# Optimization experiments

Hardware: AMD Instinct MI355X
Metric: run time of the kernel (lower is better)

## Reference

```python
import jax, jax.numpy as jnp
import numpy as np

OUT_FEATURES = 4096
IN_FEATURES = 4096
SCALE_EPS = 1e-5


def setup_inputs() -> dict:
    key = jax.random.key(0)
    k1, k2, k3 = jax.random.split(key, 3)
    x = jax.random.normal(k1, (8192, IN_FEATURES), dtype=jnp.float32)
    # packed int4 weights: two signed nibbles per byte-equivalent int
    weight_packed = jax.random.randint(k2, (OUT_FEATURES, IN_FEATURES // 2), 0, 256, dtype=jnp.int32)
    weight_scale = jax.random.uniform(k3, (OUT_FEATURES,), dtype=jnp.float32) * 0.01 + 1e-4
    return {"x": x, "weight_packed": weight_packed, "weight_scale": weight_scale}


def _unpack_int4(weight_packed):
    # low nibble first, then high nibble, sign-extended from 4 bits
    low = weight_packed & 15
    high = (weight_packed >> 4) & 15
    low = jnp.where(low > 7, low - 16, low)
    high = jnp.where(high > 7, high - 16, high)
    # interleave -> [out_features, in_features]
    w_q = jnp.stack([low, high], axis=-1).reshape(weight_packed.shape[0], -1)
    return w_q


def reference(x, weight_packed, weight_scale):
    # per-row activation quantization to int4 range [-8, 7]
    x_max = jnp.max(jnp.abs(x), axis=-1, keepdims=True)
    x_scale = jnp.maximum(x_max / 7.0, SCALE_EPS)          # [tokens, 1]
    x_q = jnp.clip(jnp.round(x / x_scale), -8.0, 7.0)      # float carrier of int4 values

    w_q = _unpack_int4(weight_packed).astype(jnp.float32)  # [out, in]

    out = jnp.einsum('ti,oi->to', x_q, w_q)                # [tokens, out]
    out = out * (x_scale * weight_scale[None, :])
    return out.astype(x.dtype)
```

## Files before the change

### kernel.cpp

```cpp
#include <hip/hip_runtime.h>

#define SCALE_EPS 1e-5f

typedef int v4i __attribute__((ext_vector_type(4)));

static __device__ __forceinline__ void gll16(const void* g, void* l) {
  __builtin_amdgcn_global_load_lds(
      (const __attribute__((address_space(1))) unsigned int*)g,
      (__attribute__((address_space(3))) unsigned int*)l,
      16, 0, 0);
}

__global__ __launch_bounds__(256) void unpack_w(const int* __restrict__ wp,
                                                char* __restrict__ wq) {
  const int kc = blockIdx.x;
  const int nt = blockIdx.y;
  const int tid = threadIdx.x;
  char* tile = wq + ((size_t)nt * 64 + kc) * 8192;
  const int n0 = nt * 128;
#pragma unroll
  for (int j = 0; j < 4; ++j) {
    int u = j * 256 + tid;
    int r = u >> 3;
    int p = u & 7;
    const v4i* src = (const v4i*)((const char*)wp + (size_t)(n0 + r) * 8192 + kc * 128 + p * 16);
    v4i v = *src;
    unsigned int b[8];
#pragma unroll
    for (int q = 0; q < 4; ++q) {
      int lo = ((v[q] & 15) ^ 8) - 8;
      int hi = (((v[q] >> 4) & 15) ^ 8) - 8;
      b[q * 2]     = (unsigned int)(lo & 255);
      b[q * 2 + 1] = (unsigned int)(hi & 255);
    }
    unsigned int w0 = b[0] | (b[1] << 8) | (b[2] << 16) | (b[3] << 24);
    unsigned int w1 = b[4] | (b[5] << 8) | (b[6] << 16) | (b[7] << 24);
    *(uint2*)(tile + (r >> 4) * 1024 + (p >> 1) * 256 + (r & 15) * 16 + (p & 1) * 8) =
        make_uint2(w0, w1);
  }
}

__global__ __launch_bounds__(256) void quant_x(const float* __restrict__ x,
                                               char* __restrict__ xq,
                                               float* __restrict__ xs) {
  __shared__ float lmax[4][4];
  const int tid = threadIdx.x;
  const int w = tid >> 6;
  const int l = tid & 63;
  const int t0 = blockIdx.x * 4;
  const int row = l >> 4;
  const int t = t0 + row;
  const int sub = l & 15;

  const float* base = x + (size_t)t * 4096 + w * 1024 + sub * 4;
  float4 vals[16];
  float m = 0.0f;
#pragma unroll
  for (int s = 0; s < 16; ++s) {
    vals[s] = *(const float4*)(base + s * 64);
    m = fmaxf(m, fmaxf(fmaxf(fabsf(vals[s].x), fabsf(vals[s].y)),
                       fmaxf(fabsf(vals[s].z), fabsf(vals[s].w))));
  }
#pragma unroll
  for (int d = 1; d < 16; d <<= 1) m = fmaxf(m, __shfl_xor(m, d, 64));
  if (sub == 0) lmax[w][row] = m;
  __syncthreads();
  float rm = fmaxf(fmaxf(lmax[0][row], lmax[1][row]),
                   fmaxf(lmax[2][row], lmax[3][row]));
  float scale = fmaxf(rm / 7.0f, SCALE_EPS);
  if (w == 0 && sub == 0) xs[t] = scale;

  const int mt = t0 >> 7;
  const int f = (t0 & 127) >> 4;
  const int r16 = t & 15;
  const int cc = sub >> 2;
  const int b4 = (sub & 3) * 4;

#pragma unroll
  for (int s = 0; s < 16; ++s) {
    float4 v = vals[s];
    int q0 = (int)fminf(fmaxf(rintf(v.x / scale), -8.0f), 7.0f);
    int q1 = (int)fminf(fmaxf(rintf(v.y / scale), -8.0f), 7.0f);
    int q2 = (int)fminf(fmaxf(rintf(v.z / scale), -8.0f), 7.0f);
    int q3 = (int)fminf(fmaxf(rintf(v.w / scale), -8.0f), 7.0f);
    unsigned int wd = (unsigned int)(q0 & 255) | ((unsigned int)(q1 & 255) << 8) |
                      ((unsigned int)(q2 & 255) << 16) | ((unsigned int)(q3 & 255) << 24);
    *(unsigned int*)(xq + ((size_t)mt * 64 + w * 16 + s) * 8192 +
                     f * 1024 + cc * 256 + r16 * 16 + b4) = wd;
  }
}

__global__ __launch_bounds__(512, 2) void gemm_i8(const char* __restrict__ xq,
                                                  const char* __restrict__ wq,
                                                  const float* __restrict__ xs,
                                                  const float* __restrict__ wsc,
                                                  float* __restrict__ out) {
  __shared__ char lds[4][32768];
  const int tid = threadIdx.x;
  const int wid = tid >> 6;
  const int lane = tid & 63;
  const int wm = wid >> 2;
  const int wn = wid & 3;

  const int bid = blockIdx.x;
  const int wg = (bid & 7) * 64 + (bid >> 3);
  const int by = wg >> 4;
  const int bx = wg & 15;

  const char* Asrc0 = xq + (size_t)(2 * by) * 64 * 8192;
  const char* Asrc1 = Asrc0 + 64 * 8192;
  const char* Bsrc0 = wq + (size_t)(2 * bx) * 64 * 8192;
  const char* Bsrc1 = Bsrc0 + 64 * 8192;
  const int toff = tid * 16;

  v4i acc[8][4] = {};
  v4i fA[2][8], fB[2][4];

#define STAGE4(kt)                                                      \
  do {                                                                  \
    char* dst_ = lds[(kt) & 3] + toff;                                  \
    gll16(Asrc0 + (size_t)(kt) * 8192 + toff, dst_);                    \
    gll16(Asrc1 + (size_t)(kt) * 8192 + toff, dst_ + 8192);             \
    gll16(Bsrc0 + (size_t)(kt) * 8192 + toff, dst_ + 16384);            \
    gll16(Bsrc1 + (size_t)(kt) * 8192 + toff, dst_ + 24576);            \
  } while (0)

#define LOADFRAGS(n, kt1)                                               \
  do {                                                                  \
    const char* As_ = lds[(kt1) & 3] + wm * 8192 + lane * 16;           \
    const char* Bs_ = lds[(kt1) & 3] + 16384 + wn * 4096 + lane * 16;   \
    _Pragma("unroll") for (int mi = 0; mi < 8; ++mi)                    \
        fA[n][mi] = *(const v4i*)(As_ + mi * 1024);                     \
    _Pragma("unroll") for (int ni = 0; ni < 4; ++ni)                    \
        fB[n][ni] = *(const v4i*)(Bs_ + ni * 1024);                     \
  } while (0)

#define MFMAC(c)                                                        \
  do {                                                                  \
    __builtin_amdgcn_s_setprio(1);                                      \
    _Pragma("unroll") for (int mi = 0; mi < 8; ++mi)                    \
        _Pragma("unroll") for (int ni = 0; ni < 4; ++ni)                \
            acc[mi][ni] = __builtin_amdgcn_mfma_i32_16x16x64_i8(        \
                fA[c][mi], fB[c][ni], acc[mi][ni], 0, 0, 0);            \
    __builtin_amdgcn_s_setprio(0);                                      \
  } while (0)

#define ITER(c, n, kt, do_stage, vm)                                    \
  do {                                                                  \
    if (do_stage) STAGE4((kt) + 3);                                     \
    LOADFRAGS(n, (kt) + 1);                                             \
    __builtin_amdgcn_sched_barrier(0);                                  \
    MFMAC(c);                                                           \
    asm volatile("s_waitcnt lgkmcnt(0)" ::: "memory");                  \
    if ((vm) == 4) asm volatile("s_waitcnt vmcnt(4)" ::: "memory");     \
    else if ((vm) == 0) asm volatile("s_waitcnt vmcnt(0)" ::: "memory");\
    __builtin_amdgcn_sched_barrier(0);                                  \
    __builtin_amdgcn_s_barrier();                                       \
    __builtin_amdgcn_sched_barrier(0);                                  \
  } while (0)

  STAGE4(0); STAGE4(1); STAGE4(2);
  asm volatile("s_waitcnt vmcnt(8)" ::: "memory");
  __builtin_amdgcn_s_barrier();
  __builtin_amdgcn_sched_barrier(0);
  LOADFRAGS(0, 0);
  asm volatile("s_waitcnt vmcnt(4) lgkmcnt(0)" ::: "memory");
  __builtin_amdgcn_sched_barrier(0);
  __builtin_amdgcn_s_barrier();
  __builtin_amdgcn_sched_barrier(0);

  for (int kt = 0; kt < 60; kt += 2) {
    ITER(0, 1, kt, true, 4);
    ITER(1, 0, kt + 1, true, 4);
  }
  ITER(0, 1, 60, true, 4);
  ITER(1, 0, 61, false, 0);
  ITER(0, 1, 62, false, -1);
  MFMAC(1);

#undef ITER
#undef MFMAC
#undef LOADFRAGS
#undef STAGE4

  float wvv[4];
#pragma unroll
  for (int ni = 0; ni < 4; ++ni)
    wvv[ni] = wsc[bx * 256 + wn * 64 + ni * 16 + (lane & 15)];
  const int rbase = by * 256 + wm * 128 + ((lane >> 4) << 2);
  const int cbase = bx * 256 + wn * 64 + (lane & 15);
#pragma unroll
  for (int mi = 0; mi < 8; ++mi) {
#pragma unroll
    for (int j = 0; j < 4; ++j) {
      int t = rbase + mi * 16 + j;
      float xsv = xs[t];
      float* orow = out + (size_t)t * 4096 + cbase;
#pragma unroll
      for (int ni = 0; ni < 4; ++ni)
        orow[ni * 16] = (float)acc[mi][ni][j] * (xsv * wvv[ni]);
    }
  }
}

extern "C" void kernel_launch(void* const* d_in, const int* in_sizes, int n_in,
                              void* d_out, int out_size, void* d_ws, size_t ws_size,
                              hipStream_t stream) {
  const float* x = (const float*)d_in[0];
  const int* wp = (const int*)d_in[1];
  const float* wsc = (const float*)d_in[2];
  float* out = (float*)d_out;
  char* ws = (char*)d_ws;

  char* xq = ws;
  char* wq = ws + 33554432;
  float* xs = (float*)(ws + 33554432 + 16777216);

  hipLaunchKernelGGL(unpack_w, dim3(64, 32), dim3(256), 0, stream, wp, wq);
  hipLaunchKernelGGL(quant_x, dim3(2048), dim3(256), 0, stream, x, xq, xs);
  hipLaunchKernelGGL(gemm_i8, dim3(512), dim3(512), 0, stream, xq, wq, xs, wsc, out);
}
```

Measured before the change: 176.0 us.

## Stream A fragments in pairs interleaved with MFMAs in the int8 GEMM loop

After: 172.8 us. Within noise of the previous version (-1.8%).

```diff
diff --git a/kernel.cpp b/kernel.cpp
--- a/kernel.cpp
+++ b/kernel.cpp
@@ -114,7 +114,8 @@
   const int toff = tid * 16;
 
   v4i acc[8][4] = {};
-  v4i fA[2][8], fB[2][4];
+  v4i fB[2][4];
+  v4i aA0, aA1, aA2, aA3;
 
 #define STAGE4(kt)                                                      \
   do {                                                                  \
@@ -125,62 +126,81 @@
     gll16(Bsrc1 + (size_t)(kt) * 8192 + toff, dst_ + 24576);            \
   } while (0)
 
-#define LOADFRAGS(n, kt1)                                               \
-  do {                                                                  \
-    const char* As_ = lds[(kt1) & 3] + wm * 8192 + lane * 16;           \
-    const char* Bs_ = lds[(kt1) & 3] + 16384 + wn * 4096 + lane * 16;   \
-    _Pragma("unroll") for (int mi = 0; mi < 8; ++mi)                    \
-        fA[n][mi] = *(const v4i*)(As_ + mi * 1024);                     \
-    _Pragma("unroll") for (int ni = 0; ni < 4; ++ni)                    \
-        fB[n][ni] = *(const v4i*)(Bs_ + ni * 1024);                     \
+#define MF2(m0, m1, x, y, c)                                                          \
+  do {                                                                                \
+    __builtin_amdgcn_s_setprio(1);                                                    \
+    _Pragma("unroll") for (int ni = 0; ni < 4; ++ni) {                                \
+      acc[m0][ni] =                                                                   \
+          __builtin_amdgcn_mfma_i32_16x16x64_i8(x, fB[c][ni], acc[m0][ni], 0, 0, 0);  \
+      acc[m1][ni] =                                                                   \
+          __builtin_amdgcn_mfma_i32_16x16x64_i8(y, fB[c][ni], acc[m1][ni], 0, 0, 0);  \
+    }                                                                                 \
+    __builtin_amdgcn_s_setprio(0);                                                    \
   } while (0)
 
-#define MFMAC(c)                                                        \
-  do {                                                                  \
-    __builtin_amdgcn_s_setprio(1);                                      \
-    _Pragma("unroll") for (int mi = 0; mi < 8; ++mi)                    \
-        _Pragma("unroll") for (int ni = 0; ni < 4; ++ni)                \
-            acc[mi][ni] = __builtin_amdgcn_mfma_i32_16x16x64_i8(        \
-                fA[c][mi], fB[c][ni], acc[mi][ni], 0, 0, 0);            \
-    __builtin_amdgcn_s_setprio(0);                                      \
-  } while (0)
-
-#define ITER(c, n, kt, do_stage, vm)                                    \
-  do {                                                                  \
-    if (do_stage) STAGE4((kt) + 3);                                     \
-    LOADFRAGS(n, (kt) + 1);                                             \
-    __builtin_amdgcn_sched_barrier(0);                                  \
-    MFMAC(c);                                                           \
-    asm volatile("s_waitcnt lgkmcnt(0)" ::: "memory");                  \
-    if ((vm) == 4) asm volatile("s_waitcnt vmcnt(4)" ::: "memory");     \
-    else if ((vm) == 0) asm volatile("s_waitcnt vmcnt(0)" ::: "memory");\
-    __builtin_amdgcn_sched_barrier(0);                                  \
-    __builtin_amdgcn_s_barrier();                                       \
-    __builtin_amdgcn_sched_barrier(0);                                  \
+#define TILE(c, kt, do_stage, do_next, vm)                                   \
+  do {                                                                       \
+    const char* As_ = lds[(kt) & 3] + wm * 8192 + lane * 16;                 \
+    const char* Bn_ = lds[((kt) + 1) & 3] + 16384 + wn * 4096 + lane * 16;   \
+    const char* An_ = lds[((kt) + 1) & 3] + wm * 8192 + lane * 16;           \
+                                 \
+    aA2 = *(const v4i*)(As_ + 2048);                                         \
+    aA3 = *(const v4i*)(As_ + 3072);                                         \
+    MF2(0, 1, aA0, aA1, c);                                                  \
+                                 \
+    aA0 = *(const v4i*)(As_ + 4096);                                         \
+    aA1 = *(const v4i*)(As_ + 5120);                                         \
+    MF2(2, 3, aA2, aA3, c);                                                  \
+                      \
+    if ((vm) == 4) asm volatile("s_waitcnt vmcnt(4)" ::: "memory");          \
+    else if ((vm) == 0) asm volatile("s_waitcnt vmcnt(0)" ::: "memory");     \
+    __builtin_amdgcn_s_barrier();                                            \
+    __builtin_amdgcn_sched_barrier(0);                                       \
+       \
+    if (do_stage) STAGE4((kt) + 3);                                          \
+    aA2 = *(const v4i*)(As_ + 6144);                                         \
+    aA3 = *(const v4i*)(As_ + 7168);                                         \
+    if (do_next) {                                                           \
+      fB[1 - (c)][0] = *(const v4i*)(Bn_);                                   \
+      fB[1 - (c)][1] = *(const v4i*)(Bn_ + 1024);                            \
+    }                                                                        \
+    MF2(4, 5, aA0, aA1, c);                                                  \
+             \
+    if (do_next) {                                                           \
+      fB[1 - (c)][2] = *(const v4i*)(Bn_ + 2048);                            \
+      fB[1 - (c)][3] = *(const v4i*)(Bn_ + 3072);                            \
+      aA0 = *(const v4i*)(An_);                                              \
+      aA1 = *(const v4i*)(An_ + 1024);                                       \
+    }                                                                        \
+    MF2(6, 7, aA2, aA3, c);                                                  \
   } while (0)
 
   STAGE4(0); STAGE4(1); STAGE4(2);
   asm volatile("s_waitcnt vmcnt(8)" ::: "memory");
   __builtin_amdgcn_s_barrier();
   __builtin_amdgcn_sched_barrier(0);
-  LOADFRAGS(0, 0);
-  asm volatile("s_waitcnt vmcnt(4) lgkmcnt(0)" ::: "memory");
-  __builtin_amdgcn_sched_barrier(0);
-  __builtin_amdgcn_s_barrier();
-  __builtin_amdgcn_sched_barrier(0);
+  {
+    const char* As_ = lds[0] + wm * 8192 + lane * 16;
+    const char* Bs_ = lds[0] + 16384 + wn * 4096 + lane * 16;
+    aA0 = *(const v4i*)(As_);
+    aA1 = *(const v4i*)(As_ + 1024);
+    fB[0][0] = *(const v4i*)(Bs_);
+    fB[0][1] = *(const v4i*)(Bs_ + 1024);
+    fB[0][2] = *(const v4i*)(Bs_ + 2048);
+    fB[0][3] = *(const v4i*)(Bs_ + 3072);
+  }
 
   for (int kt = 0; kt < 60; kt += 2) {
-    ITER(0, 1, kt, true, 4);
-    ITER(1, 0, kt + 1, true, 4);
-  }
-  ITER(0, 1, 60, true, 4);
-  ITER(1, 0, 61, false, 0);
-  ITER(0, 1, 62, false, -1);
-  MFMAC(1);
-
-#undef ITER
-#undef MFMAC
-#undef LOADFRAGS
+    TILE(0, kt, 1, 1, 4);
+    TILE(1, kt + 1, 1, 1, 4);
+  }
+  TILE(0, 60, 1, 1, 4);
+  TILE(1, 61, 0, 1, 4);
+  TILE(0, 62, 0, 1, 0);
+  TILE(1, 63, 0, 0, -1);
+
+#undef TILE
+#undef MF2
 #undef STAGE4
 
   float wvv[4];
```
